# Performance work log

Hardware: AMD Instinct MI355X
Metric: run time of the kernel (lower is better)

The kernel has to match this reference:

```python
import jax, jax.numpy as jnp
import numpy as np


def _conv(x, w, b=None, pad=0):
    # x: [B,C,H,W], w: [O,I,kh,kw]
    y = jax.lax.conv_general_dilated(
        x, w, window_strides=(1, 1), padding=[(pad, pad), (pad, pad)],
        dimension_numbers=('NCHW', 'OIHW', 'NCHW'))
    if b is not None:
        y = y + b[None, :, None, None]
    return y


def _resb(x, w1, w2):
    h = _conv(x, w1, pad=1)
    h = jax.nn.leaky_relu(h, 0.1)
    h = _conv(h, w2, pad=1)
    return h + x


def setup_inputs() -> dict:
    key = jax.random.key(0)
    ks = jax.random.split(key, 16)
    B, C, H, W, K = 2, 64, 128, 256, 16
    s = 0.05
    return {
        'x_left': jax.random.normal(ks[0], (B, C, H, W), jnp.float32),
        'x_right': jax.random.normal(ks[1], (B, C, H, W), jnp.float32),
        'xxs': jax.random.randint(ks[2], (B, H * W, K), 0, H, jnp.int32),
        'yys': jax.random.randint(ks[3], (B, H * W, K), 0, W, jnp.int32),
        'is_training': 0,
        'rb_w1': jax.random.normal(ks[4], (C, C, 3, 3), jnp.float32) * s,
        'rb_w2': jax.random.normal(ks[5], (C, C, 3, 3), jnp.float32) * s,
        'b1_w': jax.random.normal(ks[6], (C, C, 1, 1), jnp.float32) * s,
        'b1_b': jax.random.normal(ks[7], (C,), jnp.float32) * s,
        'b2_w': jax.random.normal(ks[8], (C, C, 1, 1), jnp.float32) * s,
        'b2_b': jax.random.normal(ks[9], (C,), jnp.float32) * s,
        'b3_w': jax.random.normal(ks[10], (C, C, 1, 1), jnp.float32) * s,
        'b3_b': jax.random.normal(ks[11], (C,), jnp.float32) * s,
        'fus_w': jax.random.normal(ks[12], (C, 2 * C, 1, 1), jnp.float32) * s,
        'fus_b': jax.random.normal(ks[13], (C,), jnp.float32) * s,
    }


def reference(x_left, x_right, xxs, yys, is_training,
              rb_w1, rb_w2, b1_w, b1_b, b2_w, b2_b, b3_w, b3_b, fus_w, fus_b):
    B, C, H, W = x_left.shape
    HW = H * W
    K = xxs.shape[-1]

    buf_l = _resb(x_left, rb_w1, rb_w2)
    buf_r = _resb(x_right, rb_w1, rb_w2)

    Q = _conv(buf_l, b1_w, b1_b)   # [B,C,H,W]
    S = _conv(buf_r, b2_w, b2_b)
    R = _conv(buf_r, b3_w, b3_b)

    # per-pixel gather: S[b,:,Pos_x,Pos_y] -> flat index into H*W
    flat = (xxs.astype(jnp.int32) * W + yys.astype(jnp.int32)).reshape(B, HW * K)  # [B,HW*K]
    Sf = S.reshape(B, C, HW)
    Rf = R.reshape(B, C, HW)
    Key = jnp.take_along_axis(Sf, flat[:, None, :], axis=2).reshape(B, C, HW, K)
    Val = jnp.take_along_axis(Rf, flat[:, None, :], axis=2).reshape(B, C, HW, K)

    Qv = Q.transpose(0, 2, 3, 1).reshape(B, HW, C)           # [B,HW,C]
    score = jnp.einsum('bpc,bcpk->bpk', Qv, Key)             # [B,HW,K]
    M = jax.nn.softmax(score, axis=-1)                       # [B,HW,K]
    buf = jnp.einsum('bpk,bckp->bpc', M, Val.transpose(0, 1, 3, 2))  # [B,HW,C]
    buf = buf.reshape(B, H, W, C).transpose(0, 3, 1, 2)      # [B,C,H,W]

    out = _conv(jnp.concatenate([buf, x_left], axis=1), fus_w, fus_b)
    M_right_to_left = M[:, :, None, :]                       # [B,HW,1,K] as in torch
    if is_training == 1:
        return out
    return (out, M_right_to_left)
```

## Files before the change

kernel.cpp:

```cpp
#include <hip/hip_runtime.h>

#define HH 128
#define WW 256
#define CH 64
#define HWP (HH * WW)

typedef __attribute__((ext_vector_type(8))) __bf16 bf16x8;
typedef __attribute__((ext_vector_type(16))) float float16;

__device__ __forceinline__ unsigned short f2bf(float f) {
    unsigned u = __float_as_uint(f);
    u += 0x7fffu + ((u >> 16) & 1u);
    return (unsigned short)(u >> 16);
}
__device__ __forceinline__ float bf2f(unsigned short u) {
    return __uint_as_float((unsigned)u << 16);
}

__global__ __launch_bounds__(256) void prep_w_k(
    const float* __restrict__ w1, const float* __restrict__ w2,
    const float* __restrict__ b1w, const float* __restrict__ b2w,
    const float* __restrict__ b3w, const float* __restrict__ fusw,
    unsigned short* __restrict__ wB)
{
    int e = blockIdx.x * 256 + threadIdx.x;
    if (e >= 94208) return;
    float val;
    if (e < 73728) {
        const float* w = (e < 36864) ? w1 : w2;
        int t = (e < 36864) ? e : e - 36864;
        int j = t & 7, L = (t >> 3) & 63, nb = (t >> 9) & 1, kc = t >> 10;
        int k  = kc * 16 + (L >> 5) * 8 + j;
        int n  = nb * 32 + (L & 31);
        int kd = k >> 6, ci = k & 63;
        val = w[(n * 64 + ci) * 9 + kd];
    } else {
        int t = e - 73728;
        if (t < 4096) {
            int j = t & 7, L = (t >> 3) & 63, i3 = t >> 9;
            int nt = i3 & 1, kc = i3 >> 1;
            int n = nt * 32 + (L & 31), k = kc * 16 + (L >> 5) * 8 + j;
            val = b1w[n * 64 + k];
        } else if (t < 12288) {
            t -= 4096;
            int j = t & 7, L = (t >> 3) & 63, i3 = t >> 9;
            int nt = i3 & 3, kc = i3 >> 2;
            int n = nt * 32 + (L & 31), k = kc * 16 + (L >> 5) * 8 + j;
            val = (n < 64) ? b2w[n * 64 + k] : b3w[(n - 64) * 64 + k];
        } else {
            t -= 12288;
            int j = t & 7, L = (t >> 3) & 63, i3 = t >> 9;
            int nt = i3 & 1, kc = i3 >> 1;
            int n = nt * 32 + (L & 31), k = kc * 16 + (L >> 5) * 8 + j;
            val = fusw[n * 128 + k];
        }
    }
    wB[e] = f2bf(val);
}

__global__ __launch_bounds__(256) void toT_k(
    const float* __restrict__ xl, const float* __restrict__ xr,
    unsigned short* __restrict__ XT)
{
    __shared__ __align__(16) unsigned short sT[64 * 68];
    const int tid = threadIdx.x;
    const int side = blockIdx.x >> 10;
    const int i0   = blockIdx.x & 1023;
    const int gp0  = i0 * 64;
    const int b    = gp0 >> 15;
    const int pofs = gp0 & (HWP - 1);
    const float* in = (side ? xr : xl) + (size_t)b * CH * HWP + pofs;

    for (int i = tid; i < 4096; i += 256) {
        int ci = i >> 6, px = i & 63;
        sT[px * 68 + ci] = f2bf(in[(size_t)ci * HWP + px]);
    }
    __syncthreads();
    const int px = tid >> 2, q = tid & 3;
    unsigned short* op = XT + ((size_t)(side * 2 + b) * HWP + pofs + px) * 64;
#pragma unroll
    for (int r = 0; r < 2; ++r)
        *(uint4*)&op[(q * 2 + r) * 8] = *(uint4*)&sT[px * 68 + (q * 2 + r) * 8];
}

__device__ __forceinline__ void stage_halo(
    unsigned short* sA, const unsigned short* inT, int x0, int y, int tid)
{
    for (int i = tid; i < 1584; i += 256) {
        int cell = i >> 3, j = i & 7;
        int row = cell / 66, col = cell - row * 66;
        int gy = y + row - 1, gx = x0 + col - 1;
        uint4 v = make_uint4(0, 0, 0, 0);
        if ((unsigned)gy < HH && (unsigned)gx < WW)
            v = *(const uint4*)&inT[(size_t)(gy * WW + gx) * 64 + j * 8];
        *(uint4*)&sA[(row * 66 + col) * 68 + j * 8] = v;
    }
}

__global__ __launch_bounds__(256) void conv1_k(
    const unsigned short* __restrict__ XT, const unsigned short* __restrict__ wB,
    unsigned short* __restrict__ H1T)
{
    __shared__ __align__(16) unsigned short sA[3 * 66 * 68];

    const int tid = threadIdx.x;
    const int x0  = blockIdx.x * 64;
    const int y   = blockIdx.y;
    const int sb  = blockIdx.z;
    const unsigned short* inT = XT + (size_t)sb * HWP * 64;

    stage_halo(sA, inT, x0, y, tid);
    __syncthreads();

    const int lane = tid & 63, wv = tid >> 6;
    const int mw = wv & 1, nw = wv >> 1;
    const int m = lane & 31, kg = lane >> 5;
    const int px_l = mw * 32 + m;

    float16 acc;
#pragma unroll
    for (int i = 0; i < 16; ++i) acc[i] = 0.f;

#pragma unroll
    for (int kc = 0; kc < 36; ++kc) {
        const int kd = kc >> 2, h = kc & 3;
        const int dy = kd / 3, dx = kd - dy * 3;
        bf16x8 af = *(const bf16x8*)&sA[((dy * 66 + px_l + dx) * 68) + h * 16 + kg * 8];
        bf16x8 bf = *(const bf16x8*)&wB[((kc * 2 + nw) * 64 + lane) * 8];
        acc = __builtin_amdgcn_mfma_f32_32x32x16_bf16(af, bf, acc, 0, 0, 0);
    }

    __syncthreads();
    unsigned short* sCb = sA;
    const int n = nw * 32 + (lane & 31);
#pragma unroll
    for (int r = 0; r < 16; ++r) {
        int pr = mw * 32 + (r & 3) + 8 * (r >> 2) + 4 * kg;
        float v = acc[r];
        v = v > 0.f ? v : 0.1f * v;
        sCb[pr * 68 + n] = f2bf(v);
    }
    __syncthreads();

    const int px = tid >> 2, q = tid & 3;
    unsigned short* op = H1T + ((size_t)sb * HWP + y * WW + x0 + px) * 64;
#pragma unroll
    for (int r = 0; r < 2; ++r)
        *(uint4*)&op[(q * 2 + r) * 8] = *(uint4*)&sCb[px * 68 + (q * 2 + r) * 8];
}

__global__ __launch_bounds__(256) void conv2_k(
    const unsigned short* __restrict__ H1T, const unsigned short* __restrict__ XT,
    const unsigned short* __restrict__ wB2, const unsigned short* __restrict__ wQ,
    const unsigned short* __restrict__ wSR, const float* __restrict__ b1b,
    const float* __restrict__ b2b, const float* __restrict__ b3b,
    unsigned short* __restrict__ QT, unsigned short* __restrict__ ST,
    unsigned short* __restrict__ RT)
{
    __shared__ __align__(16) unsigned short sA[3 * 66 * 68];

    const int tid = threadIdx.x;
    const int x0  = blockIdx.x * 64;
    const int y   = blockIdx.y;
    const int sb  = blockIdx.z;
    const int side = sb >> 1, b = sb & 1;
    const unsigned short* inT = H1T + (size_t)sb * HWP * 64;

    stage_halo(sA, inT, x0, y, tid);
    __syncthreads();

    const int lane = tid & 63, wv = tid >> 6;
    const int mw = wv & 1, nw = wv >> 1;
    const int m = lane & 31, kg = lane >> 5;
    const int px_l = mw * 32 + m;

    float16 acc;
#pragma unroll
    for (int i = 0; i < 16; ++i) acc[i] = 0.f;

#pragma unroll
    for (int kc = 0; kc < 36; ++kc) {
        const int kd = kc >> 2, h = kc & 3;
        const int dy = kd / 3, dx = kd - dy * 3;
        bf16x8 af = *(const bf16x8*)&sA[((dy * 66 + px_l + dx) * 68) + h * 16 + kg * 8];
        bf16x8 bf = *(const bf16x8*)&wB2[((kc * 2 + nw) * 64 + lane) * 8];
        acc = __builtin_amdgcn_mfma_f32_32x32x16_bf16(af, bf, acc, 0, 0, 0);
    }

    __syncthreads();
    unsigned short* sCb = sA;
    unsigned short* sC2 = sA + 4352;
    const int n = nw * 32 + (lane & 31);
    const unsigned short* xres = XT + (size_t)sb * HWP * 64;
#pragma unroll
    for (int r = 0; r < 16; ++r) {
        int pr = mw * 32 + (r & 3) + 8 * (r >> 2) + 4 * kg;
        float xv = bf2f(xres[(size_t)(y * WW + x0 + pr) * 64 + n]);
        sCb[pr * 68 + n] = f2bf(acc[r] + xv);
    }
    __syncthreads();

    if (side == 0) {
        float16 a2;
#pragma unroll
        for (int i = 0; i < 16; ++i) a2[i] = 0.f;
#pragma unroll
        for (int kc = 0; kc < 4; ++kc) {
            bf16x8 af = *(const bf16x8*)&sCb[px_l * 68 + kc * 16 + kg * 8];
            bf16x8 bf = *(const bf16x8*)&wQ[((kc * 2 + nw) * 64 + lane) * 8];
            a2 = __builtin_amdgcn_mfma_f32_32x32x16_bf16(af, bf, a2, 0, 0, 0);
        }
        float bv = b1b[n];
#pragma unroll
        for (int r = 0; r < 16; ++r) {
            int pr = mw * 32 + (r & 3) + 8 * (r >> 2) + 4 * kg;
            sC2[pr * 68 + n] = f2bf(a2[r] + bv);
        }
        __syncthreads();
        const int px = tid >> 2, q = tid & 3;
        unsigned short* op = QT + ((size_t)b * HWP + y * WW + x0 + px) * 64;
#pragma unroll
        for (int r = 0; r < 2; ++r)
            *(uint4*)&op[(q * 2 + r) * 8] = *(uint4*)&sC2[px * 68 + (q * 2 + r) * 8];
    } else {
        float16 a2[2];
#pragma unroll
        for (int t = 0; t < 2; ++t)
#pragma unroll
            for (int i = 0; i < 16; ++i) a2[t][i] = 0.f;
#pragma unroll
        for (int kc = 0; kc < 4; ++kc) {
            bf16x8 af = *(const bf16x8*)&sCb[px_l * 68 + kc * 16 + kg * 8];
#pragma unroll
            for (int t = 0; t < 2; ++t) {
                int nt = nw * 2 + t;
                bf16x8 bf = *(const bf16x8*)&wSR[((kc * 4 + nt) * 64 + lane) * 8];
                a2[t] = __builtin_amdgcn_mfma_f32_32x32x16_bf16(af, bf, a2[t], 0, 0, 0);
            }
        }
#pragma unroll
        for (int t = 0; t < 2; ++t) {
            int nn = (nw * 2 + t) * 32 + (lane & 31);
            float bv = (nn < 64) ? b2b[nn] : b3b[nn - 64];
#pragma unroll
            for (int r = 0; r < 16; ++r) {
                int pr = mw * 32 + (r & 3) + 8 * (r >> 2) + 4 * kg;
                sC2[pr * 132 + nn] = f2bf(a2[t][r] + bv);
            }
        }
        __syncthreads();
        const int px = tid >> 2, q = tid & 3;
        const size_t prow = (size_t)b * HWP + y * WW + x0 + px;
        unsigned short* op = ((q < 2) ? ST : RT) + prow * 64 + (q & 1) * 32;
#pragma unroll
        for (int j = 0; j < 4; ++j)
            *(uint4*)&op[j * 8] = *(uint4*)&sC2[px * 132 + q * 32 + j * 8];
    }
}

__global__ __launch_bounds__(256) void attn_k(
    const unsigned short* __restrict__ QT, const unsigned short* __restrict__ ST,
    const unsigned short* __restrict__ RT, const int* __restrict__ xxs,
    const int* __restrict__ yys, unsigned short* __restrict__ bufT,
    float* __restrict__ Mout)
{
    const int tid  = threadIdx.x;
    const int lane = tid & 63;
    const size_t gp = (size_t)blockIdx.x * 4 + (tid >> 6);
    const size_t bbase = (gp >> 15) << 15;
    const int k  = lane & 15, cq = lane >> 4;

    const int flat = xxs[gp * 16 + k] * WW + yys[gp * 16 + k];

    const unsigned short* srow = ST + (bbase + (size_t)flat) * 64 + cq * 16;
    const unsigned short* qrow = QT + gp * 64 + cq * 16;
    float s = 0.f;
#pragma unroll
    for (int h = 0; h < 2; ++h) {
        uint4 sv = *(const uint4*)(srow + h * 8);
        uint4 qv = *(const uint4*)(qrow + h * 8);
        const unsigned* sa = (const unsigned*)&sv;
        const unsigned* qa = (const unsigned*)&qv;
#pragma unroll
        for (int d = 0; d < 4; ++d) {
            s = fmaf(__uint_as_float(sa[d] << 16),
                     __uint_as_float(qa[d] << 16), s);
            s = fmaf(__uint_as_float(sa[d] & 0xffff0000u),
                     __uint_as_float(qa[d] & 0xffff0000u), s);
        }
    }
    s += __shfl_xor(s, 16, 64);
    s += __shfl_xor(s, 32, 64);

    float mx = s;
#pragma unroll
    for (int mm = 1; mm <= 8; mm <<= 1) mx = fmaxf(mx, __shfl_xor(mx, mm, 64));
    const float e = __expf(s - mx);
    float sum = e;
#pragma unroll
    for (int mm = 1; mm <= 8; mm <<= 1) sum += __shfl_xor(sum, mm, 64);
    const float mval = e * (1.f / sum);

    if (lane < 16) Mout[gp * 16 + lane] = mval;

    const unsigned short* rbase = RT + bbase * 64;
    float acc = 0.f;
#pragma unroll
    for (int kk = 0; kk < 16; ++kk) {
        int   fi = __builtin_amdgcn_readlane(flat, kk);
        float mk = __uint_as_float(
            __builtin_amdgcn_readlane(__float_as_uint(mval), kk));
        acc = fmaf(mk, bf2f(rbase[(size_t)fi * 64 + lane]), acc);
    }
    bufT[gp * 64 + lane] = f2bf(acc);
}

__global__ __launch_bounds__(256) void fuse_k(
    const unsigned short* __restrict__ bufT, const unsigned short* __restrict__ XT,
    const unsigned short* __restrict__ wfrag, const float* __restrict__ bias,
    float* __restrict__ out)
{
    __shared__ __align__(16) unsigned char smem[64 * 68 * 4];
    unsigned short* sA = (unsigned short*)smem;
    float* sC = (float*)smem;

    const int tid = threadIdx.x;
    const size_t gp0 = (size_t)blockIdx.x * 64;
    const int b    = (int)(gp0 >> 15);
    const int pofs = (int)(gp0 & (HWP - 1));
    const unsigned short* xlT = XT + ((size_t)b * HWP + pofs) * 64;

    for (int i = tid; i < 1024; i += 256) {
        int px = i >> 4, j = i & 15;
        uint4 v;
        if (j < 8) v = *(const uint4*)&bufT[(gp0 + px) * 64 + j * 8];
        else       v = *(const uint4*)&xlT[(size_t)px * 64 + (j - 8) * 8];
        *(uint4*)&sA[px * 132 + ((j < 8) ? j * 8 : 64 + (j - 8) * 8)] = v;
    }
    __syncthreads();

    const int lane = tid & 63, wv = tid >> 6;
    const int mw = wv & 1, nw = wv >> 1;
    const int m = lane & 31, kg = lane >> 5;
    const int px_l = mw * 32 + m;

    float16 acc;
#pragma unroll
    for (int i = 0; i < 16; ++i) acc[i] = 0.f;

#pragma unroll
    for (int kc = 0; kc < 8; ++kc) {
        bf16x8 af = *(const bf16x8*)&sA[px_l * 132 + kc * 16 + kg * 8];
        bf16x8 bf = *(const bf16x8*)&wfrag[((kc * 2 + nw) * 64 + lane) * 8];
        acc = __builtin_amdgcn_mfma_f32_32x32x16_bf16(af, bf, acc, 0, 0, 0);
    }
    __syncthreads();

    const int co_l = nw * 32 + (lane & 31);
#pragma unroll
    for (int r = 0; r < 16; ++r) {
        int pr = mw * 32 + (r & 3) + 8 * (r >> 2) + 4 * kg;
        sC[co_l * 68 + pr] = acc[r];
    }
    __syncthreads();

    const int co = tid >> 2, p0 = (tid & 3) * 16;
    const float bv = bias[co];
    float* op = out + ((size_t)b * CH + co) * HWP + pofs + p0;
#pragma unroll
    for (int q = 0; q < 4; ++q) {
        float4 v = *(float4*)&sC[co * 68 + p0 + q * 4];
        v.x += bv; v.y += bv; v.z += bv; v.w += bv;
        *(float4*)&op[q * 4] = v;
    }
}

extern "C" void kernel_launch(void* const* d_in, const int* in_sizes, int n_in,
                              void* d_out, int out_size, void* d_ws, size_t ws_size,
                              hipStream_t stream)
{
    const float* x_left  = (const float*)d_in[0];
    const float* x_right = (const float*)d_in[1];
    const int*   xxs     = (const int*)d_in[2];
    const int*   yys     = (const int*)d_in[3];
    const float* rb_w1   = (const float*)d_in[5];
    const float* rb_w2   = (const float*)d_in[6];
    const float* b1_w    = (const float*)d_in[7];
    const float* b1_b    = (const float*)d_in[8];
    const float* b2_w    = (const float*)d_in[9];
    const float* b2_b    = (const float*)d_in[10];
    const float* b3_w    = (const float*)d_in[11];
    const float* b3_b    = (const float*)d_in[12];
    const float* fus_w   = (const float*)d_in[13];
    const float* fus_b   = (const float*)d_in[14];

    float* out  = (float*)d_out;
    float* Mout = out + (size_t)2 * CH * HWP;

    unsigned short* ws2 = (unsigned short*)d_ws;
    unsigned short* XT   = ws2;
    unsigned short* H1T  = ws2 + 8388608;
    unsigned short* QT   = ws2 + 16777216;
    unsigned short* ST   = ws2 + 20971520;
    unsigned short* RT   = ws2 + 25165824;
    unsigned short* bufT = ws2 + 29360128;
    unsigned short* wB   = ws2 + 33554432;

    prep_w_k<<<368, 256, 0, stream>>>(rb_w1, rb_w2, b1_w, b2_w, b3_w, fus_w, wB);
    toT_k<<<2048, 256, 0, stream>>>(x_left, x_right, XT);

    dim3 cgrid(WW / 64, HH, 4), cblk(256);
    conv1_k<<<cgrid, cblk, 0, stream>>>(XT, wB, H1T);
    conv2_k<<<cgrid, cblk, 0, stream>>>(H1T, XT, wB + 36864, wB + 73728,
                                        wB + 77824, b1_b, b2_b, b3_b, QT, ST, RT);

    attn_k<<<16384, 256, 0, stream>>>(QT, ST, RT, xxs, yys, bufT, Mout);
    fuse_k<<<1024, 256, 0, stream>>>(bufT, XT, wB + 86016, fus_b, out);
}
```

Baseline: 201.9 us.

## Widen conv tiles to 128 pixels so each wave reuses weight fragments twice

The conv1 and conv2 kernels now process 128-pixel row tiles instead of 64. Each wave computes two 32-pixel M tiles that share one global weight fragment load per K step. This halves weight reloads and halo overhead per pixel. In exchange, shared memory per block roughly doubles, accumulator register use doubles, and the grid has half as many blocks, which may lower occupancy.

```diff
diff --git a/kernel.cpp b/kernel.cpp
--- a/kernel.cpp
+++ b/kernel.cpp
@@ -83,17 +83,17 @@
         *(uint4*)&op[(q * 2 + r) * 8] = *(uint4*)&sT[px * 68 + (q * 2 + r) * 8];
 }
 
-__device__ __forceinline__ void stage_halo(
+__device__ __forceinline__ void stage_halo130(
     unsigned short* sA, const unsigned short* inT, int x0, int y, int tid)
 {
-    for (int i = tid; i < 1584; i += 256) {
+    for (int i = tid; i < 3120; i += 256) {
         int cell = i >> 3, j = i & 7;
-        int row = cell / 66, col = cell - row * 66;
+        int row = cell / 130, col = cell - row * 130;
         int gy = y + row - 1, gx = x0 + col - 1;
         uint4 v = make_uint4(0, 0, 0, 0);
         if ((unsigned)gy < HH && (unsigned)gx < WW)
             v = *(const uint4*)&inT[(size_t)(gy * WW + gx) * 64 + j * 8];
-        *(uint4*)&sA[(row * 66 + col) * 68 + j * 8] = v;
+        *(uint4*)&sA[(row * 130 + col) * 68 + j * 8] = v;
     }
 }
 
@@ -101,33 +101,35 @@
     const unsigned short* __restrict__ XT, const unsigned short* __restrict__ wB,
     unsigned short* __restrict__ H1T)
 {
-    __shared__ __align__(16) unsigned short sA[3 * 66 * 68];
+    __shared__ __align__(16) unsigned short sA[3 * 130 * 68];
 
     const int tid = threadIdx.x;
-    const int x0  = blockIdx.x * 64;
+    const int x0  = blockIdx.x * 128;
     const int y   = blockIdx.y;
     const int sb  = blockIdx.z;
     const unsigned short* inT = XT + (size_t)sb * HWP * 64;
 
-    stage_halo(sA, inT, x0, y, tid);
+    stage_halo130(sA, inT, x0, y, tid);
     __syncthreads();
 
     const int lane = tid & 63, wv = tid >> 6;
-    const int mw = wv & 1, nw = wv >> 1;
+    const int h = wv & 1, nw = wv >> 1;
     const int m = lane & 31, kg = lane >> 5;
-    const int px_l = mw * 32 + m;
-
-    float16 acc;
-#pragma unroll
-    for (int i = 0; i < 16; ++i) acc[i] = 0.f;
+
+    float16 acc0, acc1;
+#pragma unroll
+    for (int i = 0; i < 16; ++i) { acc0[i] = 0.f; acc1[i] = 0.f; }
 
 #pragma unroll
     for (int kc = 0; kc < 36; ++kc) {
-        const int kd = kc >> 2, h = kc & 3;
+        const int kd = kc >> 2, hh = kc & 3;
         const int dy = kd / 3, dx = kd - dy * 3;
-        bf16x8 af = *(const bf16x8*)&sA[((dy * 66 + px_l + dx) * 68) + h * 16 + kg * 8];
-        bf16x8 bf = *(const bf16x8*)&wB[((kc * 2 + nw) * 64 + lane) * 8];
-        acc = __builtin_amdgcn_mfma_f32_32x32x16_bf16(af, bf, acc, 0, 0, 0);
+        bf16x8 bfg = *(const bf16x8*)&wB[((kc * 2 + nw) * 64 + lane) * 8];
+        const int base = (dy * 130 + h * 64 + m + dx) * 68 + hh * 16 + kg * 8;
+        bf16x8 af0 = *(const bf16x8*)&sA[base];
+        bf16x8 af1 = *(const bf16x8*)&sA[base + 32 * 68];
+        acc0 = __builtin_amdgcn_mfma_f32_32x32x16_bf16(af0, bfg, acc0, 0, 0, 0);
+        acc1 = __builtin_amdgcn_mfma_f32_32x32x16_bf16(af1, bfg, acc1, 0, 0, 0);
     }
 
     __syncthreads();
@@ -135,18 +137,19 @@
     const int n = nw * 32 + (lane & 31);
 #pragma unroll
     for (int r = 0; r < 16; ++r) {
-        int pr = mw * 32 + (r & 3) + 8 * (r >> 2) + 4 * kg;
-        float v = acc[r];
-        v = v > 0.f ? v : 0.1f * v;
-        sCb[pr * 68 + n] = f2bf(v);
-    }
-    __syncthreads();
-
-    const int px = tid >> 2, q = tid & 3;
-    unsigned short* op = H1T + ((size_t)sb * HWP + y * WW + x0 + px) * 64;
-#pragma unroll
-    for (int r = 0; r < 2; ++r)
-        *(uint4*)&op[(q * 2 + r) * 8] = *(uint4*)&sCb[px * 68 + (q * 2 + r) * 8];
+        int pr = h * 64 + (r & 3) + 8 * (r >> 2) + 4 * kg;
+        float v0 = acc0[r]; v0 = v0 > 0.f ? v0 : 0.1f * v0;
+        float v1 = acc1[r]; v1 = v1 > 0.f ? v1 : 0.1f * v1;
+        sCb[pr * 68 + n] = f2bf(v0);
+        sCb[(pr + 32) * 68 + n] = f2bf(v1);
+    }
+    __syncthreads();
+
+    const int px = tid >> 1, q = tid & 1;
+    unsigned short* op = H1T + ((size_t)sb * HWP + y * WW + x0 + px) * 64 + q * 32;
+#pragma unroll
+    for (int j = 0; j < 4; ++j)
+        *(uint4*)&op[j * 8] = *(uint4*)&sCb[px * 68 + q * 32 + j * 8];
 }
 
 __global__ __launch_bounds__(256) void conv2_k(
@@ -157,85 +160,94 @@
     unsigned short* __restrict__ QT, unsigned short* __restrict__ ST,
     unsigned short* __restrict__ RT)
 {
-    __shared__ __align__(16) unsigned short sA[3 * 66 * 68];
+    __shared__ __align__(16) unsigned short sA[3 * 130 * 68];
 
     const int tid = threadIdx.x;
-    const int x0  = blockIdx.x * 64;
+    const int x0  = blockIdx.x * 128;
     const int y   = blockIdx.y;
     const int sb  = blockIdx.z;
     const int side = sb >> 1, b = sb & 1;
     const unsigned short* inT = H1T + (size_t)sb * HWP * 64;
 
-    stage_halo(sA, inT, x0, y, tid);
+    stage_halo130(sA, inT, x0, y, tid);
     __syncthreads();
 
     const int lane = tid & 63, wv = tid >> 6;
-    const int mw = wv & 1, nw = wv >> 1;
+    const int h = wv & 1, nw = wv >> 1;
     const int m = lane & 31, kg = lane >> 5;
-    const int px_l = mw * 32 + m;
-
-    float16 acc;
-#pragma unroll
-    for (int i = 0; i < 16; ++i) acc[i] = 0.f;
+
+    float16 acc0, acc1;
+#pragma unroll
+    for (int i = 0; i < 16; ++i) { acc0[i] = 0.f; acc1[i] = 0.f; }
 
 #pragma unroll
     for (int kc = 0; kc < 36; ++kc) {
-        const int kd = kc >> 2, h = kc & 3;
+        const int kd = kc >> 2, hh = kc & 3;
         const int dy = kd / 3, dx = kd - dy * 3;
-        bf16x8 af = *(const bf16x8*)&sA[((dy * 66 + px_l + dx) * 68) + h * 16 + kg * 8];
-        bf16x8 bf = *(const bf16x8*)&wB2[((kc * 2 + nw) * 64 + lane) * 8];
-        acc = __builtin_amdgcn_mfma_f32_32x32x16_bf16(af, bf, acc, 0, 0, 0);
+        bf16x8 bfg = *(const bf16x8*)&wB2[((kc * 2 + nw) * 64 + lane) * 8];
+        const int base = (dy * 130 + h * 64 + m + dx) * 68 + hh * 16 + kg * 8;
+        bf16x8 af0 = *(const bf16x8*)&sA[base];
+        bf16x8 af1 = *(const bf16x8*)&sA[base + 32 * 68];
+        acc0 = __builtin_amdgcn_mfma_f32_32x32x16_bf16(af0, bfg, acc0, 0, 0, 0);
+        acc1 = __builtin_amdgcn_mfma_f32_32x32x16_bf16(af1, bfg, acc1, 0, 0, 0);
     }
 
     __syncthreads();
     unsigned short* sCb = sA;
-    unsigned short* sC2 = sA + 4352;
+    unsigned short* sC2 = sA + 8704;
     const int n = nw * 32 + (lane & 31);
-    const unsigned short* xres = XT + (size_t)sb * HWP * 64;
+    const unsigned short* xres = XT + ((size_t)sb * HWP + y * WW + x0) * 64;
 #pragma unroll
     for (int r = 0; r < 16; ++r) {
-        int pr = mw * 32 + (r & 3) + 8 * (r >> 2) + 4 * kg;
-        float xv = bf2f(xres[(size_t)(y * WW + x0 + pr) * 64 + n]);
-        sCb[pr * 68 + n] = f2bf(acc[r] + xv);
+        int pr = h * 64 + (r & 3) + 8 * (r >> 2) + 4 * kg;
+        float xv0 = bf2f(xres[(size_t)pr * 64 + n]);
+        float xv1 = bf2f(xres[(size_t)(pr + 32) * 64 + n]);
+        sCb[pr * 68 + n] = f2bf(acc0[r] + xv0);
+        sCb[(pr + 32) * 68 + n] = f2bf(acc1[r] + xv1);
     }
     __syncthreads();
 
     if (side == 0) {
-        float16 a2;
-#pragma unroll
-        for (int i = 0; i < 16; ++i) a2[i] = 0.f;
+        float16 a0, a1;
+#pragma unroll
+        for (int i = 0; i < 16; ++i) { a0[i] = 0.f; a1[i] = 0.f; }
 #pragma unroll
         for (int kc = 0; kc < 4; ++kc) {
-            bf16x8 af = *(const bf16x8*)&sCb[px_l * 68 + kc * 16 + kg * 8];
-            bf16x8 bf = *(const bf16x8*)&wQ[((kc * 2 + nw) * 64 + lane) * 8];
-            a2 = __builtin_amdgcn_mfma_f32_32x32x16_bf16(af, bf, a2, 0, 0, 0);
+            bf16x8 bfg = *(const bf16x8*)&wQ[((kc * 2 + nw) * 64 + lane) * 8];
+            bf16x8 af0 = *(const bf16x8*)&sCb[(h * 64 + m) * 68 + kc * 16 + kg * 8];
+            bf16x8 af1 = *(const bf16x8*)&sCb[(h * 64 + 32 + m) * 68 + kc * 16 + kg * 8];
+            a0 = __builtin_amdgcn_mfma_f32_32x32x16_bf16(af0, bfg, a0, 0, 0, 0);
+            a1 = __builtin_amdgcn_mfma_f32_32x32x16_bf16(af1, bfg, a1, 0, 0, 0);
         }
         float bv = b1b[n];
 #pragma unroll
         for (int r = 0; r < 16; ++r) {
-            int pr = mw * 32 + (r & 3) + 8 * (r >> 2) + 4 * kg;
-            sC2[pr * 68 + n] = f2bf(a2[r] + bv);
+            int pr = h * 64 + (r & 3) + 8 * (r >> 2) + 4 * kg;
+            sC2[pr * 68 + n] = f2bf(a0[r] + bv);
+            sC2[(pr + 32) * 68 + n] = f2bf(a1[r] + bv);
         }
         __syncthreads();
-        const int px = tid >> 2, q = tid & 3;
-        unsigned short* op = QT + ((size_t)b * HWP + y * WW + x0 + px) * 64;
-#pragma unroll
-        for (int r = 0; r < 2; ++r)
-            *(uint4*)&op[(q * 2 + r) * 8] = *(uint4*)&sC2[px * 68 + (q * 2 + r) * 8];
+        const int px = tid >> 1, q = tid & 1;
+        unsigned short* op = QT + ((size_t)b * HWP + y * WW + x0 + px) * 64 + q * 32;
+#pragma unroll
+        for (int j = 0; j < 4; ++j)
+            *(uint4*)&op[j * 8] = *(uint4*)&sC2[px * 68 + q * 32 + j * 8];
     } else {
-        float16 a2[2];
+        float16 a0[2], a1[2];
 #pragma unroll
         for (int t = 0; t < 2; ++t)
 #pragma unroll
-            for (int i = 0; i < 16; ++i) a2[t][i] = 0.f;
+            for (int i = 0; i < 16; ++i) { a0[t][i] = 0.f; a1[t][i] = 0.f; }
 #pragma unroll
         for (int kc = 0; kc < 4; ++kc) {
-            bf16x8 af = *(const bf16x8*)&sCb[px_l * 68 + kc * 16 + kg * 8];
+            bf16x8 af0 = *(const bf16x8*)&sCb[(h * 64 + m) * 68 + kc * 16 + kg * 8];
+            bf16x8 af1 = *(const bf16x8*)&sCb[(h * 64 + 32 + m) * 68 + kc * 16 + kg * 8];
 #pragma unroll
             for (int t = 0; t < 2; ++t) {
                 int nt = nw * 2 + t;
-                bf16x8 bf = *(const bf16x8*)&wSR[((kc * 4 + nt) * 64 + lane) * 8];
-                a2[t] = __builtin_amdgcn_mfma_f32_32x32x16_bf16(af, bf, a2[t], 0, 0, 0);
+                bf16x8 bfg = *(const bf16x8*)&wSR[((kc * 4 + nt) * 64 + lane) * 8];
+                a0[t] = __builtin_amdgcn_mfma_f32_32x32x16_bf16(af0, bfg, a0[t], 0, 0, 0);
+                a1[t] = __builtin_amdgcn_mfma_f32_32x32x16_bf16(af1, bfg, a1[t], 0, 0, 0);
             }
         }
 #pragma unroll
@@ -244,17 +256,18 @@
             float bv = (nn < 64) ? b2b[nn] : b3b[nn - 64];
 #pragma unroll
             for (int r = 0; r < 16; ++r) {
-                int pr = mw * 32 + (r & 3) + 8 * (r >> 2) + 4 * kg;
-                sC2[pr * 132 + nn] = f2bf(a2[t][r] + bv);
+                int pr = h * 64 + (r & 3) + 8 * (r >> 2) + 4 * kg;
+                sC2[pr * 132 + nn] = f2bf(a0[t][r] + bv);
+                sC2[(pr + 32) * 132 + nn] = f2bf(a1[t][r] + bv);
             }
         }
         __syncthreads();
-        const int px = tid >> 2, q = tid & 3;
+        const int px = tid >> 1, q = tid & 1;
         const size_t prow = (size_t)b * HWP + y * WW + x0 + px;
-        unsigned short* op = ((q < 2) ? ST : RT) + prow * 64 + (q & 1) * 32;
-#pragma unroll
-        for (int j = 0; j < 4; ++j)
-            *(uint4*)&op[j * 8] = *(uint4*)&sC2[px * 132 + q * 32 + j * 8];
+        unsigned short* op = (q ? RT : ST) + prow * 64;
+#pragma unroll
+        for (int j = 0; j < 8; ++j)
+            *(uint4*)&op[j * 8] = *(uint4*)&sC2[px * 132 + q * 64 + j * 8];
     }
 }
 
@@ -276,9 +289,9 @@
     const unsigned short* qrow = QT + gp * 64 + cq * 16;
     float s = 0.f;
 #pragma unroll
-    for (int h = 0; h < 2; ++h) {
-        uint4 sv = *(const uint4*)(srow + h * 8);
-        uint4 qv = *(const uint4*)(qrow + h * 8);
+    for (int hh = 0; hh < 2; ++hh) {
+        uint4 sv = *(const uint4*)(srow + hh * 8);
+        uint4 qv = *(const uint4*)(qrow + hh * 8);
         const unsigned* sa = (const unsigned*)&sv;
         const unsigned* qa = (const unsigned*)&qv;
 #pragma unroll
@@ -409,7 +422,7 @@
     prep_w_k<<<368, 256, 0, stream>>>(rb_w1, rb_w2, b1_w, b2_w, b3_w, fus_w, wB);
     toT_k<<<2048, 256, 0, stream>>>(x_left, x_right, XT);
 
-    dim3 cgrid(WW / 64, HH, 4), cblk(256);
+    dim3 cgrid(WW / 128, HH, 4), cblk(256);
     conv1_k<<<cgrid, cblk, 0, stream>>>(XT, wB, H1T);
     conv2_k<<<cgrid, cblk, 0, stream>>>(H1T, XT, wB + 36864, wB + 73728,
                                         wB + 77824, b1_b, b2_b, b3_b, QT, ST, RT);
```

Measured after the change: 213.3 us. 1.06x slower.

## Fuse gather-attention and fusion 1x1 conv into one kernel

Applied to the files above, without the earlier changes.

Merges the attention kernel and the fusion conv kernel so each block of 512 threads computes the attention output for 64 pixels into shared memory and then runs the MFMA 1x1 conv directly. This removes the bufT global round trip and one kernel launch. The block-to-pixel mapping interleaves the two batches across blocks. The cost is that each wave now handles 8 pixels serially instead of 1, which lowers the parallelism available to hide gather latency, and only half of the threads run the MFMA stage.

```diff
diff --git a/kernel.cpp b/kernel.cpp
--- a/kernel.cpp
+++ b/kernel.cpp
@@ -258,120 +258,126 @@
     }
 }
 
-__global__ __launch_bounds__(256) void attn_k(
+__global__ __launch_bounds__(512) void attn_fuse_k(
     const unsigned short* __restrict__ QT, const unsigned short* __restrict__ ST,
     const unsigned short* __restrict__ RT, const int* __restrict__ xxs,
-    const int* __restrict__ yys, unsigned short* __restrict__ bufT,
-    float* __restrict__ Mout)
-{
+    const int* __restrict__ yys, const unsigned short* __restrict__ XT,
+    const unsigned short* __restrict__ wfrag, const float* __restrict__ bias,
+    float* __restrict__ out, float* __restrict__ Mout)
+{
+    __shared__ __align__(16) unsigned char smem[64 * 68 * 4];
+    unsigned short* sBuf = (unsigned short*)smem;
+    unsigned short* sXT  = (unsigned short*)smem + 64 * 68;
+    float*          sC   = (float*)smem;
+
     const int tid  = threadIdx.x;
     const int lane = tid & 63;
-    const size_t gp = (size_t)blockIdx.x * 4 + (tid >> 6);
-    const size_t bbase = (gp >> 15) << 15;
-    const int k  = lane & 15, cq = lane >> 4;
-
-    const int flat = xxs[gp * 16 + k] * WW + yys[gp * 16 + k];
-
-    const unsigned short* srow = ST + (bbase + (size_t)flat) * 64 + cq * 16;
-    const unsigned short* qrow = QT + gp * 64 + cq * 16;
-    float s = 0.f;
-#pragma unroll
-    for (int h = 0; h < 2; ++h) {
-        uint4 sv = *(const uint4*)(srow + h * 8);
-        uint4 qv = *(const uint4*)(qrow + h * 8);
-        const unsigned* sa = (const unsigned*)&sv;
-        const unsigned* qa = (const unsigned*)&qv;
-#pragma unroll
-        for (int d = 0; d < 4; ++d) {
-            s = fmaf(__uint_as_float(sa[d] << 16),
-                     __uint_as_float(qa[d] << 16), s);
-            s = fmaf(__uint_as_float(sa[d] & 0xffff0000u),
-                     __uint_as_float(qa[d] & 0xffff0000u), s);
-        }
-    }
-    s += __shfl_xor(s, 16, 64);
-    s += __shfl_xor(s, 32, 64);
-
-    float mx = s;
-#pragma unroll
-    for (int mm = 1; mm <= 8; mm <<= 1) mx = fmaxf(mx, __shfl_xor(mx, mm, 64));
-    const float e = __expf(s - mx);
-    float sum = e;
-#pragma unroll
-    for (int mm = 1; mm <= 8; mm <<= 1) sum += __shfl_xor(sum, mm, 64);
-    const float mval = e * (1.f / sum);
-
-    if (lane < 16) Mout[gp * 16 + lane] = mval;
-
-    const unsigned short* rbase = RT + bbase * 64;
-    float acc = 0.f;
-#pragma unroll
-    for (int kk = 0; kk < 16; ++kk) {
-        int   fi = __builtin_amdgcn_readlane(flat, kk);
-        float mk = __uint_as_float(
-            __builtin_amdgcn_readlane(__float_as_uint(mval), kk));
-        acc = fmaf(mk, bf2f(rbase[(size_t)fi * 64 + lane]), acc);
-    }
-    bufT[gp * 64 + lane] = f2bf(acc);
-}
-
-__global__ __launch_bounds__(256) void fuse_k(
-    const unsigned short* __restrict__ bufT, const unsigned short* __restrict__ XT,
-    const unsigned short* __restrict__ wfrag, const float* __restrict__ bias,
-    float* __restrict__ out)
-{
-    __shared__ __align__(16) unsigned char smem[64 * 68 * 4];
-    unsigned short* sA = (unsigned short*)smem;
-    float* sC = (float*)smem;
-
-    const int tid = threadIdx.x;
-    const size_t gp0 = (size_t)blockIdx.x * 64;
-    const int b    = (int)(gp0 >> 15);
-    const int pofs = (int)(gp0 & (HWP - 1));
-    const unsigned short* xlT = XT + ((size_t)b * HWP + pofs) * 64;
-
-    for (int i = tid; i < 1024; i += 256) {
-        int px = i >> 4, j = i & 15;
-        uint4 v;
-        if (j < 8) v = *(const uint4*)&bufT[(gp0 + px) * 64 + j * 8];
-        else       v = *(const uint4*)&xlT[(size_t)px * 64 + (j - 8) * 8];
-        *(uint4*)&sA[px * 132 + ((j < 8) ? j * 8 : 64 + (j - 8) * 8)] = v;
-    }
-    __syncthreads();
-
-    const int lane = tid & 63, wv = tid >> 6;
-    const int mw = wv & 1, nw = wv >> 1;
+    const int wv   = tid >> 6;
+
+    const int blk = blockIdx.x;
+    const int b   = (blk & 4) ? 1 : 0;
+    const int sub = (blk >> 3) * 4 + (blk & 3);
+    const int pofs = sub * 64;
+    const size_t gp0   = (size_t)b * HWP + pofs;
+    const size_t bbase = (size_t)b * HWP;
+
+    {
+        const unsigned short* xlT = XT + gp0 * 64;
+        int px = tid >> 3, j = tid & 7;
+        *(uint4*)&sXT[px * 68 + j * 8] = *(const uint4*)&xlT[(size_t)px * 64 + j * 8];
+    }
+
+    const int k = lane & 15, cq = lane >> 4;
+    for (int it = 0; it < 8; ++it) {
+        const int pl = wv * 8 + it;
+        const size_t gp = gp0 + pl;
+
+        const int flat = xxs[gp * 16 + k] * WW + yys[gp * 16 + k];
+
+        const unsigned short* srow = ST + (bbase + (size_t)flat) * 64 + cq * 16;
+        const unsigned short* qrow = QT + gp * 64 + cq * 16;
+        float s = 0.f;
+#pragma unroll
+        for (int hh = 0; hh < 2; ++hh) {
+            uint4 sv = *(const uint4*)(srow + hh * 8);
+            uint4 qv = *(const uint4*)(qrow + hh * 8);
+            const unsigned* sa = (const unsigned*)&sv;
+            const unsigned* qa = (const unsigned*)&qv;
+#pragma unroll
+            for (int d = 0; d < 4; ++d) {
+                s = fmaf(__uint_as_float(sa[d] << 16),
+                         __uint_as_float(qa[d] << 16), s);
+                s = fmaf(__uint_as_float(sa[d] & 0xffff0000u),
+                         __uint_as_float(qa[d] & 0xffff0000u), s);
+            }
+        }
+        s += __shfl_xor(s, 16, 64);
+        s += __shfl_xor(s, 32, 64);
+
+        float mx = s;
+#pragma unroll
+        for (int mm = 1; mm <= 8; mm <<= 1) mx = fmaxf(mx, __shfl_xor(mx, mm, 64));
+        const float e = __expf(s - mx);
+        float sum = e;
+#pragma unroll
+        for (int mm = 1; mm <= 8; mm <<= 1) sum += __shfl_xor(sum, mm, 64);
+        const float mval = e * (1.f / sum);
+
+        if (lane < 16) Mout[gp * 16 + lane] = mval;
+
+        const unsigned short* rbase = RT + bbase * 64;
+        float acc = 0.f;
+#pragma unroll
+        for (int kk = 0; kk < 16; ++kk) {
+            int   fi = __builtin_amdgcn_readlane(flat, kk);
+            float mk = __uint_as_float(
+                __builtin_amdgcn_readlane(__float_as_uint(mval), kk));
+            acc = fmaf(mk, bf2f(rbase[(size_t)fi * 64 + lane]), acc);
+        }
+        sBuf[pl * 68 + lane] = f2bf(acc);
+    }
+    __syncthreads();
+
+    float16 facc;
+#pragma unroll
+    for (int i = 0; i < 16; ++i) facc[i] = 0.f;
+    const int mw = wv & 1, nw = (wv >> 1) & 1;
     const int m = lane & 31, kg = lane >> 5;
     const int px_l = mw * 32 + m;
 
-    float16 acc;
-#pragma unroll
-    for (int i = 0; i < 16; ++i) acc[i] = 0.f;
-
-#pragma unroll
-    for (int kc = 0; kc < 8; ++kc) {
-        bf16x8 af = *(const bf16x8*)&sA[px_l * 132 + kc * 16 + kg * 8];
-        bf16x8 bf = *(const bf16x8*)&wfrag[((kc * 2 + nw) * 64 + lane) * 8];
-        acc = __builtin_amdgcn_mfma_f32_32x32x16_bf16(af, bf, acc, 0, 0, 0);
-    }
-    __syncthreads();
-
-    const int co_l = nw * 32 + (lane & 31);
-#pragma unroll
-    for (int r = 0; r < 16; ++r) {
-        int pr = mw * 32 + (r & 3) + 8 * (r >> 2) + 4 * kg;
-        sC[co_l * 68 + pr] = acc[r];
-    }
-    __syncthreads();
-
-    const int co = tid >> 2, p0 = (tid & 3) * 16;
-    const float bv = bias[co];
-    float* op = out + ((size_t)b * CH + co) * HWP + pofs + p0;
-#pragma unroll
-    for (int q = 0; q < 4; ++q) {
-        float4 v = *(float4*)&sC[co * 68 + p0 + q * 4];
-        v.x += bv; v.y += bv; v.z += bv; v.w += bv;
-        *(float4*)&op[q * 4] = v;
+    if (tid < 256) {
+#pragma unroll
+        for (int kc = 0; kc < 8; ++kc) {
+            const unsigned short* asrc = (kc < 4)
+                ? &sBuf[px_l * 68 + kc * 16 + kg * 8]
+                : &sXT[px_l * 68 + (kc - 4) * 16 + kg * 8];
+            bf16x8 af = *(const bf16x8*)asrc;
+            bf16x8 bf = *(const bf16x8*)&wfrag[((kc * 2 + nw) * 64 + lane) * 8];
+            facc = __builtin_amdgcn_mfma_f32_32x32x16_bf16(af, bf, facc, 0, 0, 0);
+        }
+    }
+    __syncthreads();
+
+    if (tid < 256) {
+        const int co_l = nw * 32 + (lane & 31);
+#pragma unroll
+        for (int r = 0; r < 16; ++r) {
+            int pr = mw * 32 + (r & 3) + 8 * (r >> 2) + 4 * kg;
+            sC[co_l * 68 + pr] = facc[r];
+        }
+    }
+    __syncthreads();
+
+    if (tid < 256) {
+        const int co = tid >> 2, p0 = (tid & 3) * 16;
+        const float bv = bias[co];
+        float* op = out + ((size_t)b * CH + co) * HWP + pofs + p0;
+#pragma unroll
+        for (int q = 0; q < 4; ++q) {
+            float4 v = *(float4*)&sC[co * 68 + p0 + q * 4];
+            v.x += bv; v.y += bv; v.z += bv; v.w += bv;
+            *(float4*)&op[q * 4] = v;
+        }
     }
 }
 
@@ -403,8 +409,7 @@
     unsigned short* QT   = ws2 + 16777216;
     unsigned short* ST   = ws2 + 20971520;
     unsigned short* RT   = ws2 + 25165824;
-    unsigned short* bufT = ws2 + 29360128;
-    unsigned short* wB   = ws2 + 33554432;
+    unsigned short* wB   = ws2 + 29360128;
 
     prep_w_k<<<368, 256, 0, stream>>>(rb_w1, rb_w2, b1_w, b2_w, b3_w, fus_w, wB);
     toT_k<<<2048, 256, 0, stream>>>(x_left, x_right, XT);
@@ -414,6 +419,6 @@
     conv2_k<<<cgrid, cblk, 0, stream>>>(H1T, XT, wB + 36864, wB + 73728,
                                         wB + 77824, b1_b, b2_b, b3_b, QT, ST, RT);
 
-    attn_k<<<16384, 256, 0, stream>>>(QT, ST, RT, xxs, yys, bufT, Mout);
-    fuse_k<<<1024, 256, 0, stream>>>(bufT, XT, wB + 86016, fus_b, out);
-}
+    attn_fuse_k<<<1024, 512, 0, stream>>>(QT, ST, RT, xxs, yys, XT,
+                                          wB + 86016, fus_b, out, Mout);
+}
```

Result: faster. 196.2 us (-2.8%).
